# Kernel optimization log

Measured on AMD Instinct MI355X. Metric: run time of the kernel, lower is better.

The kernel has to match this reference:

```python
import jax, jax.numpy as jnp
import numpy as np

ALPHA = 0.2  # leaky relu slope

def setup_inputs() -> dict:
    key = jax.random.key(0)
    k1, k2, k3, k4 = jax.random.split(key, 4)
    b, n, din, dout = 8, 2048, 256, 128
    x = jax.random.normal(k1, (b, n, din), dtype=jnp.float32)
    adj = jax.random.randint(k2, (b, n, n), 0, 2, dtype=jnp.int32)
    # xavier-ish scaling for params
    W = jax.random.normal(k3, (dout, din), dtype=jnp.float32) * (1.414 * (2.0 / (din + dout)) ** 0.5)
    a = jax.random.normal(k4, (2 * dout,), dtype=jnp.float32) * (1.414 * (2.0 / (2 * dout + 1)) ** 0.5)
    return {"x": x, "adj": adj, "W": W, "a": a}

def reference(x, adj, W, a):
    # x: [b, n, din]; W: [dout, din]; a: [2*dout]
    wh = jnp.einsum('bnd,od->bno', x, W)           # [b, n, dout]
    dout = W.shape[0]
    a_src, a_dst = a[:dout], a[dout:]
    # e_ij = leaky_relu(a_src . wh_i + a_dst . wh_j)  (decomposed, avoids O(n^2 * 2d) concat)
    e = (wh @ a_src)[:, :, None] + (wh @ a_dst)[:, None, :]  # [b, n, n]
    e = jnp.where(e >= 0, e, ALPHA * e)
    e = jnp.where(adj != 0, e, -jnp.inf)
    attention = jax.nn.softmax(e, axis=2)          # [b, n, n]
    out = jnp.einsum('bij,bjo->bio', attention, wh)  # [b, n, dout]
    return jax.nn.relu(out)
```

## Files before the change

### kernel.cpp

```cpp
#include <hip/hip_runtime.h>
#include <hip/hip_bf16.h>
#include <stdint.h>

#define GAT_ALPHA 0.2f
#define LOG2E 1.4426950408889634f

typedef __attribute__((ext_vector_type(8))) __bf16 bf16x8;
typedef __attribute__((ext_vector_type(4))) float f32x4;

union B8 {
  bf16x8 b;
  unsigned short u[8];
  unsigned int w[4];
  int4 i4;
};

__device__ __forceinline__ unsigned int pk2bf(float lo, float hi) {
  union { __hip_bfloat162 h; unsigned int u; } cv;
  cv.h = __float22bfloat162_rn(make_float2(lo, hi));
  return cv.u;
}

__device__ __forceinline__ void dma16(const void* g, void* l) {
  __builtin_amdgcn_global_load_lds(
      (const __attribute__((address_space(1))) unsigned int*)g,
      (__attribute__((address_space(3))) unsigned int*)l, 16, 0, 0);
}

__global__ __launch_bounds__(256, 2) void gat_wh(
    const float* __restrict__ x, const float* __restrict__ W,
    const float* __restrict__ a, unsigned short* __restrict__ whTf,
    float* __restrict__ s_out, float* __restrict__ d_out) {
  __shared__ unsigned short WF[8][4][512];
  const int tid = threadIdx.x;
  const int wave = tid >> 6, lane = tid & 63;
  const int il = lane & 15, quad = lane >> 4;
  const int row0 = blockIdx.x * 64;
  const int i = row0 + wave * 16 + il;
  B8 av[8];
  {
    const float* xp = x + (size_t)i * 256 + quad * 8;
#pragma unroll
    for (int kc = 0; kc < 8; ++kc) {
      float4 lo = *(const float4*)(xp + kc * 32);
      float4 hi = *(const float4*)(xp + kc * 32 + 4);
      av[kc].w[0] = pk2bf(lo.x, lo.y);
      av[kc].w[1] = pk2bf(lo.z, lo.w);
      av[kc].w[2] = pk2bf(hi.x, hi.y);
      av[kc].w[3] = pk2bf(hi.z, hi.w);
    }
  }
  f32x4 acc[8];
#pragma unroll
  for (int nt = 0; nt < 8; ++nt) acc[nt] = (f32x4){0.f, 0.f, 0.f, 0.f};
#pragma unroll
  for (int h = 0; h < 2; ++h) {
    if (h) __syncthreads();
#pragma unroll
    for (int p = 0; p < 16; ++p) {
      const int f = p * 1024 + tid * 4;
      const int o = f >> 7, kk = f & 127;
      float4 v = *(const float4*)(W + o * 256 + h * 128 + kk);
      uint2 pk;
      pk.x = pk2bf(v.x, v.y);
      pk.y = pk2bf(v.z, v.w);
      *(uint2*)(&WF[o >> 4][kk >> 5][((o & 15) + (((kk & 31) >> 3) << 4)) * 8 + (kk & 7)]) = pk;
    }
    __syncthreads();
#pragma unroll
    for (int kl = 0; kl < 4; ++kl) {
      const int kc = h * 4 + kl;
#pragma unroll
      for (int nt = 0; nt < 8; ++nt) {
        B8 bv;
        bv.i4 = *(const int4*)(&WF[nt][kl][lane * 8]);
        acc[nt] = __builtin_amdgcn_mfma_f32_16x16x32_bf16(av[kc].b, bv.b, acc[nt], 0, 0, 0);
      }
    }
  }
  float asrc[8], adst[8];
#pragma unroll
  for (int nt = 0; nt < 8; ++nt) {
    asrc[nt] = a[nt * 16 + il];
    adst[nt] = a[128 + nt * 16 + il];
  }
  float sp[4], dp[4];
#pragma unroll
  for (int r = 0; r < 4; ++r) {
    float sv = 0.f, dv = 0.f;
#pragma unroll
    for (int nt = 0; nt < 8; ++nt) {
      sv += acc[nt][r] * asrc[nt];
      dv += acc[nt][r] * adst[nt];
    }
    sp[r] = sv; dp[r] = dv;
  }
#pragma unroll
  for (int off = 1; off <= 8; off <<= 1) {
#pragma unroll
    for (int r = 0; r < 4; ++r) {
      sp[r] += __shfl_xor(sp[r], off, 64);
      dp[r] += __shfl_xor(dp[r], off, 64);
    }
  }
  if (il == 0) {
#pragma unroll
    for (int r = 0; r < 4; ++r) {
      s_out[row0 + wave * 16 + quad * 4 + r] = sp[r];
      d_out[row0 + wave * 16 + quad * 4 + r] = dp[r];
    }
  }
  const int b = row0 >> 11;
  const int jc = ((row0 & 2047) >> 5) + (wave >> 1);
  const int kin = ((wave & 1) << 4) + (quad << 2);
  const int kq = kin >> 3, u0 = kin & 7;
#pragma unroll
  for (int nt = 0; nt < 8; ++nt) {
    uint2 pk;
    pk.x = pk2bf(acc[nt][0], acc[nt][1]);
    pk.y = pk2bf(acc[nt][2], acc[nt][3]);
    *(uint2*)(whTf + ((((size_t)(b * 64 + jc)) * 8 + nt) << 9) + ((il + (kq << 4)) << 3) + u0) = pk;
  }
}

__global__ __launch_bounds__(256) void gat_attn(
    const int* __restrict__ adj, const unsigned short* __restrict__ whTf,
    const float* __restrict__ s, const float* __restrict__ dvec,
    float* __restrict__ out) {
  __shared__ unsigned short vbuf[2][2][8][512];
  __shared__ float dl[2048];
  const int tid = threadIdx.x;
  const int wave = tid >> 6;
  const int lane = tid & 63;
  const int il = lane & 15;
  const int quad = lane >> 4;
  const int qo = quad << 3;
  const int b = blockIdx.x & 7;
  const int tile = blockIdx.x >> 3;
  const int rbase = tile * 64;
  {
    const float* dsrc = dvec + ((size_t)b << 11);
#pragma unroll
    for (int it = 0; it < 2; ++it) {
      const int idx = it * 1024 + tid * 4;
      float4 v = *(const float4*)(dsrc + idx);
      v.x *= LOG2E; v.y *= LOG2E; v.z *= LOG2E; v.w *= LOG2E;
      *(float4*)(&dl[idx]) = v;
    }
  }
  const int* aro = adj + ((((size_t)b << 11) + rbase + wave * 16) << 11);
  int lv[16];
#pragma unroll
  for (int r = 0; r < 16; ++r) lv[r] = aro[(r << 11) + lane];
  const unsigned short* whTb = whTf + (((size_t)b * 64) << 12);
  {
#pragma unroll
    for (int h = 0; h < 2; ++h) {
      const int nt = wave * 2 + h;
      dma16(whTb + ((size_t)(0 * 8 + nt) << 9) + (lane << 3), &vbuf[0][0][nt][0]);
      dma16(whTb + ((size_t)(1 * 8 + nt) << 9) + (lane << 3), &vbuf[0][1][nt][0]);
    }
  }
  const int i = rbase + wave * 16 + il;
  const size_t browi = ((size_t)b << 11) + i;
  const float svL = s[browi] * LOG2E;
  unsigned long long mcur;
  {
    unsigned long long sel = __ballot(lv[0] != 0);
#pragma unroll
    for (int r = 1; r < 16; ++r) {
      const unsigned long long mm = __ballot(lv[r] != 0);
      sel = (il == r) ? mm : sel;
    }
    mcur = sel;
  }
  f32x4 acc[8];
#pragma unroll
  for (int nt = 0; nt < 8; ++nt) acc[nt] = (f32x4){0.f, 0.f, 0.f, 0.f};
  float den = 0.f;
  __syncthreads();

  for (int T = 0; T < 32; ++T) {
    const int cur = T & 1, nxt = cur ^ 1;
    if (T < 31) {
#pragma unroll
      for (int r = 0; r < 16; ++r) lv[r] = aro[(r << 11) + (T + 1) * 64 + lane];
#pragma unroll
      for (int h = 0; h < 2; ++h) {
        const int nt = wave * 2 + h;
        dma16(whTb + (((size_t)(2 * T + 2) * 8 + nt) << 9) + (lane << 3), &vbuf[nxt][0][nt][0]);
        dma16(whTb + (((size_t)(2 * T + 3) * 8 + nt) << 9) + (lane << 3), &vbuf[nxt][1][nt][0]);
      }
    }
#pragma unroll
    for (int c = 0; c < 2; ++c) {
      const int j0 = (2 * T + c) * 32;
      const unsigned int mq = (unsigned int)(mcur >> (32 * c + qo));
      const float4 d0 = *(const float4*)(&dl[j0 + qo]);
      const float4 d1 = *(const float4*)(&dl[j0 + qo + 4]);
      const float dd[8] = {d0.x, d0.y, d0.z, d0.w, d1.x, d1.y, d1.z, d1.w};
      B8 af[8];
#pragma unroll
      for (int nt = 0; nt < 8; ++nt)
        af[nt].i4 = *(const int4*)((const char*)&vbuf[cur][c][nt][0] + lane * 16);
      float pv[8];
#pragma unroll
      for (int u = 0; u < 8; ++u) {
        float t0 = svL + dd[u];
        float e2 = fmaxf(t0, GAT_ALPHA * t0);
        float p = __builtin_amdgcn_exp2f(e2);
        p = ((mq >> u) & 1u) ? p : 0.f;
        den += p;
        pv[u] = p;
      }
      B8 pf;
      pf.w[0] = pk2bf(pv[0], pv[1]);
      pf.w[1] = pk2bf(pv[2], pv[3]);
      pf.w[2] = pk2bf(pv[4], pv[5]);
      pf.w[3] = pk2bf(pv[6], pv[7]);
#pragma unroll
      for (int nt = 0; nt < 8; ++nt)
        acc[nt] = __builtin_amdgcn_mfma_f32_16x16x32_bf16(af[nt].b, pf.b, acc[nt], 0, 0, 0);
    }
    if (T < 31) {
      unsigned long long sel = __ballot(lv[0] != 0);
#pragma unroll
      for (int r = 1; r < 16; ++r) {
        const unsigned long long mm = __ballot(lv[r] != 0);
        sel = (il == r) ? mm : sel;
      }
      mcur = sel;
    }
    __syncthreads();
  }
  den += __shfl_xor(den, 16, 64);
  den += __shfl_xor(den, 32, 64);
  const float inv = 1.0f / den;
  float* op = out + browi * 128;
#pragma unroll
  for (int nt = 0; nt < 8; ++nt) {
    float4 v;
    v.x = fmaxf(acc[nt][0] * inv, 0.f);
    v.y = fmaxf(acc[nt][1] * inv, 0.f);
    v.z = fmaxf(acc[nt][2] * inv, 0.f);
    v.w = fmaxf(acc[nt][3] * inv, 0.f);
    *(float4*)(op + nt * 16 + quad * 4) = v;
  }
}

extern "C" void kernel_launch(void* const* d_in, const int* in_sizes, int n_in,
                              void* d_out, int out_size, void* d_ws, size_t ws_size,
                              hipStream_t stream) {
  const float* x = (const float*)d_in[0];
  const int* adj = (const int*)d_in[1];
  const float* W = (const float*)d_in[2];
  const float* a = (const float*)d_in[3];
  float* out = (float*)d_out;
  unsigned short* whTf = (unsigned short*)d_ws;
  float* s = (float*)((char*)d_ws + (size_t)4 * 1024 * 1024);
  float* dv = s + 16384;
  gat_wh<<<256, 256, 0, stream>>>(x, W, a, whTf, s, dv);
  gat_attn<<<256, 256, 0, stream>>>(adj, whTf, s, dv, out);
}
```

Before: 235.4 us.

## Deepen adjacency prefetch to two tiles with manual unroll and partial vmcnt waits

The attention loop is unrolled by two with ping-pong register sets for adjacency rows, so adjacency loads run two tiles ahead instead of one. The full __syncthreads is replaced by an inline s_waitcnt vmcnt(16) plus s_barrier, so the wave waits only for the older DMA and loads rather than every outstanding global load. This aims to hide global-memory latency on the dominant adj stream. In exchange it uses more registers (three 16-int arrays) and depends on a hand-counted vmcnt value, which is fragile if the compiler reorders loads.

```diff
diff --git a/kernel.cpp b/kernel.cpp
--- a/kernel.cpp
+++ b/kernel.cpp
@@ -122,6 +122,54 @@
     *(uint2*)(whTf + ((((size_t)(b * 64 + jc)) * 8 + nt) << 9) + ((il + (kq << 4)) << 3) + u0) = pk;
   }
 }
+
+#define ATTN_COMPUTE(Tval, CUR)                                                    \
+  _Pragma("unroll") for (int c = 0; c < 2; ++c) {                                  \
+    const int j0 = (2 * (Tval) + c) * 32;                                          \
+    const unsigned int mq = (unsigned int)(mcur >> (32 * c + qo));                 \
+    const float4 d0 = *(const float4*)(&dl[j0 + qo]);                              \
+    const float4 d1 = *(const float4*)(&dl[j0 + qo + 4]);                          \
+    const float dd[8] = {d0.x, d0.y, d0.z, d0.w, d1.x, d1.y, d1.z, d1.w};          \
+    B8 af[8];                                                                      \
+    _Pragma("unroll") for (int nt = 0; nt < 8; ++nt)                               \
+        af[nt].i4 = *(const int4*)((const char*)&vbuf[CUR][c][nt][0] + lane * 16); \
+    float pv[8];                                                                   \
+    _Pragma("unroll") for (int u = 0; u < 8; ++u) {                                \
+      float t0 = svL + dd[u];                                                      \
+      float e2 = fmaxf(t0, GAT_ALPHA * t0);                                        \
+      float p = __builtin_amdgcn_exp2f(e2);                                        \
+      p = ((mq >> u) & 1u) ? p : 0.f;                                              \
+      den += p;                                                                    \
+      pv[u] = p;                                                                   \
+    }                                                                              \
+    B8 pf;                                                                         \
+    pf.w[0] = pk2bf(pv[0], pv[1]);                                                 \
+    pf.w[1] = pk2bf(pv[2], pv[3]);                                                 \
+    pf.w[2] = pk2bf(pv[4], pv[5]);                                                 \
+    pf.w[3] = pk2bf(pv[6], pv[7]);                                                 \
+    _Pragma("unroll") for (int nt = 0; nt < 8; ++nt)                               \
+      acc[nt] = __builtin_amdgcn_mfma_f32_16x16x32_bf16(af[nt].b, pf.b,            \
+                                                        acc[nt], 0, 0, 0);         \
+  }
+
+#define ATTN_BALLOT(LVC)                                                           \
+  {                                                                                \
+    unsigned long long sel = __ballot(LVC[0] != 0);                                \
+    _Pragma("unroll") for (int r = 1; r < 16; ++r) {                               \
+      const unsigned long long mm = __ballot(LVC[r] != 0);                         \
+      sel = (il == r) ? mm : sel;                                                  \
+    }                                                                              \
+    mcur = sel;                                                                    \
+  }
+
+#define ATTN_DMA(PAIR, NXT)                                                        \
+  _Pragma("unroll") for (int h = 0; h < 2; ++h) {                                  \
+    const int nt = wave * 2 + h;                                                   \
+    dma16(whTb + (((size_t)(2 * (PAIR)) * 8 + nt) << 9) + (lane << 3),             \
+          &vbuf[NXT][0][nt][0]);                                                   \
+    dma16(whTb + (((size_t)(2 * (PAIR) + 1) * 8 + nt) << 9) + (lane << 3),         \
+          &vbuf[NXT][1][nt][0]);                                                   \
+  }
 
 __global__ __launch_bounds__(256) void gat_attn(
     const int* __restrict__ adj, const unsigned short* __restrict__ whTf,
@@ -149,90 +197,54 @@
     }
   }
   const int* aro = adj + ((((size_t)b << 11) + rbase + wave * 16) << 11);
-  int lv[16];
-#pragma unroll
-  for (int r = 0; r < 16; ++r) lv[r] = aro[(r << 11) + lane];
+  int lv0[16], lvA[16], lvB[16];
+#pragma unroll
+  for (int r = 0; r < 16; ++r) lv0[r] = aro[(r << 11) + lane];
+#pragma unroll
+  for (int r = 0; r < 16; ++r) lvA[r] = aro[(r << 11) + 64 + lane];
   const unsigned short* whTb = whTf + (((size_t)b * 64) << 12);
-  {
-#pragma unroll
-    for (int h = 0; h < 2; ++h) {
-      const int nt = wave * 2 + h;
-      dma16(whTb + ((size_t)(0 * 8 + nt) << 9) + (lane << 3), &vbuf[0][0][nt][0]);
-      dma16(whTb + ((size_t)(1 * 8 + nt) << 9) + (lane << 3), &vbuf[0][1][nt][0]);
-    }
-  }
+  ATTN_DMA(0, 0);
   const int i = rbase + wave * 16 + il;
   const size_t browi = ((size_t)b << 11) + i;
   const float svL = s[browi] * LOG2E;
-  unsigned long long mcur;
-  {
-    unsigned long long sel = __ballot(lv[0] != 0);
-#pragma unroll
-    for (int r = 1; r < 16; ++r) {
-      const unsigned long long mm = __ballot(lv[r] != 0);
-      sel = (il == r) ? mm : sel;
-    }
-    mcur = sel;
-  }
   f32x4 acc[8];
 #pragma unroll
   for (int nt = 0; nt < 8; ++nt) acc[nt] = (f32x4){0.f, 0.f, 0.f, 0.f};
   float den = 0.f;
+  unsigned long long mcur;
+  ATTN_BALLOT(lv0);
   __syncthreads();
 
-  for (int T = 0; T < 32; ++T) {
-    const int cur = T & 1, nxt = cur ^ 1;
-    if (T < 31) {
-#pragma unroll
-      for (int r = 0; r < 16; ++r) lv[r] = aro[(r << 11) + (T + 1) * 64 + lane];
-#pragma unroll
-      for (int h = 0; h < 2; ++h) {
-        const int nt = wave * 2 + h;
-        dma16(whTb + (((size_t)(2 * T + 2) * 8 + nt) << 9) + (lane << 3), &vbuf[nxt][0][nt][0]);
-        dma16(whTb + (((size_t)(2 * T + 3) * 8 + nt) << 9) + (lane << 3), &vbuf[nxt][1][nt][0]);
-      }
-    }
-#pragma unroll
-    for (int c = 0; c < 2; ++c) {
-      const int j0 = (2 * T + c) * 32;
-      const unsigned int mq = (unsigned int)(mcur >> (32 * c + qo));
-      const float4 d0 = *(const float4*)(&dl[j0 + qo]);
-      const float4 d1 = *(const float4*)(&dl[j0 + qo + 4]);
-      const float dd[8] = {d0.x, d0.y, d0.z, d0.w, d1.x, d1.y, d1.z, d1.w};
-      B8 af[8];
-#pragma unroll
-      for (int nt = 0; nt < 8; ++nt)
-        af[nt].i4 = *(const int4*)((const char*)&vbuf[cur][c][nt][0] + lane * 16);
-      float pv[8];
-#pragma unroll
-      for (int u = 0; u < 8; ++u) {
-        float t0 = svL + dd[u];
-        float e2 = fmaxf(t0, GAT_ALPHA * t0);
-        float p = __builtin_amdgcn_exp2f(e2);
-        p = ((mq >> u) & 1u) ? p : 0.f;
-        den += p;
-        pv[u] = p;
-      }
-      B8 pf;
-      pf.w[0] = pk2bf(pv[0], pv[1]);
-      pf.w[1] = pk2bf(pv[2], pv[3]);
-      pf.w[2] = pk2bf(pv[4], pv[5]);
-      pf.w[3] = pk2bf(pv[6], pv[7]);
-#pragma unroll
-      for (int nt = 0; nt < 8; ++nt)
-        acc[nt] = __builtin_amdgcn_mfma_f32_16x16x32_bf16(af[nt].b, pf.b, acc[nt], 0, 0, 0);
-    }
-    if (T < 31) {
-      unsigned long long sel = __ballot(lv[0] != 0);
-#pragma unroll
-      for (int r = 1; r < 16; ++r) {
-        const unsigned long long mm = __ballot(lv[r] != 0);
-        sel = (il == r) ? mm : sel;
-      }
-      mcur = sel;
-    }
-    __syncthreads();
-  }
+  for (int t2 = 0; t2 < 15; ++t2) {
+    const int T0 = 2 * t2;
+    {
+      ATTN_DMA(T0 + 1, 1);
+      __builtin_amdgcn_sched_barrier(0);
+#pragma unroll
+      for (int r = 0; r < 16; ++r) lvB[r] = aro[(r << 11) + (T0 + 2) * 64 + lane];
+      ATTN_COMPUTE(T0, 0);
+      ATTN_BALLOT(lvA);
+      asm volatile("s_waitcnt vmcnt(16)\n\ts_barrier" ::: "memory");
+    }
+    {
+      const int T1 = T0 + 1;
+      ATTN_DMA(T1 + 1, 0);
+      __builtin_amdgcn_sched_barrier(0);
+#pragma unroll
+      for (int r = 0; r < 16; ++r) lvA[r] = aro[(r << 11) + (T1 + 2) * 64 + lane];
+      ATTN_COMPUTE(T1, 1);
+      ATTN_BALLOT(lvB);
+      asm volatile("s_waitcnt vmcnt(16)\n\ts_barrier" ::: "memory");
+    }
+  }
+  {
+    ATTN_DMA(31, 1);
+    ATTN_COMPUTE(30, 0);
+    ATTN_BALLOT(lvA);
+    asm volatile("s_waitcnt vmcnt(0)\n\ts_barrier" ::: "memory");
+  }
+  ATTN_COMPUTE(31, 1);
+
   den += __shfl_xor(den, 16, 64);
   den += __shfl_xor(den, 32, 64);
   const float inv = 1.0f / den;
```

New measurement: 237.6 us. About the same (+0.9%).
